# Kernel tuning notes

Hardware: AMD Instinct MI355X
Metric: run time of the kernel (lower is better)

## Reference

```python
import jax, jax.numpy as jnp
import numpy as np

EMBED_DIM = 1024
NUM_HEADS = 16
HEAD_DIM = EMBED_DIM // NUM_HEADS


def setup_inputs() -> dict:
    key = jax.random.key(0)
    ks = jax.random.split(key, 9)
    B, S, D = 2, 2048, EMBED_DIM
    scale = 1.0 / np.sqrt(D)
    x = jax.random.normal(ks[0], (B, S, D), dtype=jnp.float32)
    # nn.Linear weights are stored as (out, in); y = x @ W.T + b
    Wq = jax.random.uniform(ks[1], (D, D), jnp.float32, -scale, scale)
    bq = jax.random.uniform(ks[2], (D,), jnp.float32, -scale, scale)
    Wk = jax.random.uniform(ks[3], (D, D), jnp.float32, -scale, scale)
    bk = jax.random.uniform(ks[4], (D,), jnp.float32, -scale, scale)
    Wv = jax.random.uniform(ks[5], (D, D), jnp.float32, -scale, scale)
    bv = jax.random.uniform(ks[6], (D,), jnp.float32, -scale, scale)
    Wo = jax.random.uniform(ks[7], (D, D), jnp.float32, -scale, scale)
    bo = jax.random.uniform(ks[8], (D,), jnp.float32, -scale, scale)
    return {"x": x, "Wq": Wq, "bq": bq, "Wk": Wk, "bk": bk,
            "Wv": Wv, "bv": bv, "Wo": Wo, "bo": bo}


def reference(x, Wq, bq, Wk, bk, Wv, bv, Wo, bo):
    B, S, D = x.shape
    H, Hd = NUM_HEADS, HEAD_DIM

    def split_heads(t):  # [B,S,D] -> [B,H,S,Hd]
        return t.reshape(B, S, H, Hd).transpose(0, 2, 1, 3)

    Q = split_heads(x @ Wq.T + bq)
    K = split_heads(x @ Wk.T + bk)
    V = split_heads(x @ Wv.T + bv)

    scores = jnp.einsum('bhqd,bhkd->bhqk', Q, K) / jnp.sqrt(
        jnp.asarray(Hd, dtype=x.dtype))
    attn = jax.nn.softmax(scores, axis=-1)
    out = jnp.einsum('bhqk,bhkd->bhqd', attn, V)  # [B,H,S,Hd]
    out = out.transpose(0, 2, 1, 3).reshape(B, S, D)
    return out @ Wo.T + bo
```

## Files before the change

kernel.cpp:

```cpp
#include <hip/hip_runtime.h>
#include <hip/hip_bf16.h>
#include <stdint.h>

typedef __attribute__((ext_vector_type(8))) short short8;
typedef __attribute__((ext_vector_type(4))) float f32x4;
typedef unsigned short u16;
typedef unsigned int u32;

static constexpr int S = 2048;
static constexpr int H = 16;
static constexpr int HD = 64;

__device__ __forceinline__ float fast_exp2(float x){
  return __builtin_amdgcn_exp2f(x);
}

__device__ __forceinline__ u16 f2bf(float f){
  union { float f; u32 u; } x; x.f = f;
  u32 r = x.u + 0x7fffu + ((x.u >> 16) & 1u);
  return (u16)(r >> 16);
}

__device__ __forceinline__ u32 cvt_pk_bf16(float lo, float hi){
  u32 r;
  asm("v_cvt_pk_bf16_f32 %0, %1, %2" : "=v"(r) : "v"(lo), "v"(hi));
  return r;
}

__global__ __launch_bounds__(256) void cast_all(const float* __restrict__ x,
                                                const float* __restrict__ Wq,
                                                const float* __restrict__ Wk,
                                                const float* __restrict__ Wv,
                                                const float* __restrict__ Wo,
                                                u16* __restrict__ xb,
                                                u16* __restrict__ Wb){
  int i = (blockIdx.x * 256 + threadIdx.x) * 4;
  const float* s; u16* d; int off;
  if (i < 4194304){
    s = x; d = xb; off = i;
  } else {
    int j = i - 4194304;
    int w = j >> 20;
    s = (w == 0) ? Wq : (w == 1) ? Wk : (w == 2) ? Wv : Wo;
    d = Wb + (w << 20);
    off = j & 1048575;
  }
  float4 v = *(const float4*)(s + off);
  ushort4 o;
  o.x = f2bf(v.x); o.y = f2bf(v.y); o.z = f2bf(v.z); o.w = f2bf(v.w);
  *(ushort4*)(d + off) = o;
}

__device__ __forceinline__ void gload_lds16(const void* g, void* lds_uniform){
  __builtin_amdgcn_global_load_lds(
      (const __attribute__((address_space(1))) u32*)g,
      (__attribute__((address_space(3))) u32*)lds_uniform,
      16, 0, 0);
}

__global__ __launch_bounds__(256) void gemm_qkv(const u16* __restrict__ A,
                                                const u16* __restrict__ Wall,
                                                const float* __restrict__ b0p,
                                                const float* __restrict__ b1p,
                                                const float* __restrict__ b2p,
                                                u16* __restrict__ obf){
  __shared__ __align__(16) u16 As[128*32];
  __shared__ __align__(16) u16 Bs[128*32];

  const int tid  = threadIdx.x;
  const int lane = tid & 63;
  const int wid  = tid >> 6;
  const int wm = wid >> 1, wn = wid & 1;
  const int l4 = lane >> 4, l15 = lane & 15;

  const int L = blockIdx.x + 8*blockIdx.y + 256*blockIdx.z;
  const int W = (L & 7)*96 + (L >> 3);
  const int z = W >> 8;
  const int rem = W & 255;
  const int n0 = (rem & 7) * 128;
  const int m0 = (rem >> 3) * 128;

  const u16* Bw = Wall + (size_t)z * (1024*1024);
  const float* bias = (z == 0) ? b0p : ((z == 1) ? b1p : b2p);

  f32x4 acc[4][4];
  #pragma unroll
  for (int m=0;m<4;m++)
    #pragma unroll
    for (int n=0;n<4;n++) acc[m][n] = (f32x4){0.f,0.f,0.f,0.f};

  const char* Ab = (const char*)A  + (size_t)m0 * 2048;
  const char* Bb = (const char*)Bw + (size_t)n0 * 2048;
  char* AsB = (char*)As;
  char* BsB = (char*)Bs;

  int ldsu[2], row_[2], col_[2];
  #pragma unroll
  for (int p=0;p<2;p++){
    ldsu[p] = wid*1024 + p*4096;
    int b = ldsu[p] + lane*16;
    row_[p] = b >> 6;
    col_[p] = b & 63;
  }

  for (int kt = 0; kt < 32; ++kt){
    const int kb = kt * 64;
    #pragma unroll
    for (int p=0;p<2;p++){
      gload_lds16(Ab + (size_t)row_[p]*2048 + kb + col_[p], AsB + ldsu[p]);
      gload_lds16(Bb + (size_t)row_[p]*2048 + kb + col_[p], BsB + ldsu[p]);
    }
    __syncthreads();

    short8 af[4], bfr[4];
    const int kcol = 8 * l4;
    #pragma unroll
    for (int m=0;m<4;m++)
      af[m] = *(const short8*)&As[(wm*64 + m*16 + l15)*32 + kcol];
    #pragma unroll
    for (int n=0;n<4;n++)
      bfr[n] = *(const short8*)&Bs[(wn*64 + n*16 + l15)*32 + kcol];

    #pragma unroll
    for (int m=0;m<4;m++)
      #pragma unroll
      for (int n=0;n<4;n++)
        acc[m][n] = __builtin_amdgcn_mfma_f32_16x16x32_bf16(af[m], bfr[n], acc[m][n], 0,0,0);

    __syncthreads();
  }

  #pragma unroll
  for (int m=0;m<4;m++){
    const int rgb = m0 + wm*64 + m*16 + 4*l4;
    #pragma unroll
    for (int n=0;n<4;n++){
      const int cg = n0 + wn*64 + n*16 + l15;
      const float bb = bias[cg];
      const int bi = rgb >> 11, si = rgb & 2047;
      const int hi = cg >> 6,  hd = cg & 63;
      if (z == 2){
        u16* outz = obf + (size_t)2 * 4194304u;
        ushort4 o;
        o.x = f2bf(acc[m][n][0] + bb);
        o.y = f2bf(acc[m][n][1] + bb);
        o.z = f2bf(acc[m][n][2] + bb);
        o.w = f2bf(acc[m][n][3] + bb);
        *(ushort4*)&outz[(((size_t)(bi*16 + hi))*64 + hd)*2048 + si] = o;
      } else {
        u16* outz = obf + (size_t)z * 4194304u;
        const float sc = (z == 0) ? 0.18033688011112042f : 1.0f;
        #pragma unroll
        for (int r=0;r<4;r++)
          outz[(((size_t)(bi*16 + hi))*2048 + (si + r))*64 + hd] =
              f2bf((acc[m][n][r] + bb) * sc);
      }
    }
  }
}

__global__ __launch_bounds__(256) void gemm_out(const u16* __restrict__ A,
                                                const u16* __restrict__ Wo,
                                                const float* __restrict__ bo,
                                                float* __restrict__ ofp){
  __shared__ __align__(16) u16 As[64*32];
  __shared__ __align__(16) u16 Bs[128*32];

  const int tid  = threadIdx.x;
  const int lane = tid & 63;
  const int wid  = tid >> 6;
  const int wm = wid >> 1, wn = wid & 1;
  const int l4 = lane >> 4, l15 = lane & 15;

  const int L = blockIdx.x + 8*blockIdx.y;
  const int W = (L & 7)*64 + (L >> 3);
  const int n0 = (W & 7) * 128;
  const int m0 = (W >> 3) * 64;

  f32x4 acc[2][4];
  #pragma unroll
  for (int m=0;m<2;m++)
    #pragma unroll
    for (int n=0;n<4;n++) acc[m][n] = (f32x4){0.f,0.f,0.f,0.f};

  const char* Ab = (const char*)A  + (size_t)m0 * 2048;
  const char* Bb = (const char*)Wo + (size_t)n0 * 2048;
  char* AsB = (char*)As;
  char* BsB = (char*)Bs;

  const int ldsuA = wid*1024;
  int rowA, colA;
  { int b = ldsuA + lane*16; rowA = b >> 6; colA = b & 63; }
  int ldsuB[2], rowB[2], colB[2];
  #pragma unroll
  for (int p=0;p<2;p++){
    ldsuB[p] = wid*2048 + p*1024;
    int b = ldsuB[p] + lane*16;
    rowB[p] = b >> 6; colB[p] = b & 63;
  }

  for (int kt = 0; kt < 32; ++kt){
    const int kb = kt * 64;
    gload_lds16(Ab + (size_t)rowA*2048 + kb + colA, AsB + ldsuA);
    #pragma unroll
    for (int p=0;p<2;p++)
      gload_lds16(Bb + (size_t)rowB[p]*2048 + kb + colB[p], BsB + ldsuB[p]);
    __syncthreads();

    short8 af[2], bfr[4];
    const int kcol = 8 * l4;
    #pragma unroll
    for (int m=0;m<2;m++)
      af[m] = *(const short8*)&As[(wm*32 + m*16 + l15)*32 + kcol];
    #pragma unroll
    for (int n=0;n<4;n++)
      bfr[n] = *(const short8*)&Bs[(wn*64 + n*16 + l15)*32 + kcol];

    #pragma unroll
    for (int m=0;m<2;m++)
      #pragma unroll
      for (int n=0;n<4;n++)
        acc[m][n] = __builtin_amdgcn_mfma_f32_16x16x32_bf16(af[m], bfr[n], acc[m][n], 0,0,0);

    __syncthreads();
  }

  #pragma unroll
  for (int m=0;m<2;m++){
    const int rgb = m0 + wm*32 + m*16 + 4*l4;
    #pragma unroll
    for (int n=0;n<4;n++){
      const int cg = n0 + wn*64 + n*16 + l15;
      const float bb = bo[cg];
      #pragma unroll
      for (int r=0;r<4;r++)
        ofp[(size_t)(rgb + r)*1024 + cg] = acc[m][n][r] + bb;
    }
  }
}

__global__ __launch_bounds__(256) void attn_fwd(const u16* __restrict__ Qg,
                                                const u16* __restrict__ Kg,
                                                const u16* __restrict__ Vtg,
                                                u16* __restrict__ Og){
  __shared__ __align__(16) u16 Ks[2*64*64];
  __shared__ __align__(16) u16 Vs[2*64*64];
  __shared__ __align__(16) u16 Ps[4*16*64];

  const int tid  = threadIdx.x;
  const int lane = tid & 63;
  const int wid  = tid >> 6;
  const int l4 = lane >> 4, l15 = lane & 15;
  const int swz = l15 & 7;

  const int L = blockIdx.x + 32*blockIdx.y;
  const int W = (L & 7)*128 + (L >> 3);
  const int qb = W & 31;
  const int bh = W >> 5;
  const size_t hoff = (size_t)bh * (S * HD);

  short8 aq0, aq1;
  {
    const u16* qp = Qg + hoff + (size_t)(qb*64 + wid*16 + l15) * HD;
    aq0 = *(const short8*)(qp + 8*l4);
    aq1 = *(const short8*)(qp + 32 + 8*l4);
  }

  const float FM = 12.0f;
  float lr = 0.f;
  f32x4 oacc[4];
  #pragma unroll
  for (int hb=0;hb<4;hb++) oacc[hb] = (f32x4){0.f,0.f,0.f,0.f};

  const char* Kb = (const char*)(Kg  + hoff);
  const char* Vb = (const char*)(Vtg + hoff);
  char* KsB = (char*)Ks;
  char* VsB = (char*)Vs;
  char* PsB = (char*)Ps + wid*2048;

  int ldsu[2], srcK[2], srcV[2];
  #pragma unroll
  for (int p=0;p<2;p++){
    ldsu[p] = wid*2048 + p*1024;
    int b   = ldsu[p] + lane*16;
    int row = b >> 7, cc = (b >> 4) & 7;
    int ccs = cc ^ (row & 7);
    srcK[p] = row*128  + (ccs << 4);
    srcV[p] = row*4096 + (ccs << 4);
  }

  #pragma unroll
  for (int p=0;p<2;p++){
    gload_lds16(Kb + srcK[p], KsB + ldsu[p]);
    gload_lds16(Vb + srcV[p], VsB + ldsu[p]);
  }
  __syncthreads();

  #pragma unroll 2
  for (int kt = 0; kt < S/64; ++kt){
    const int cur = kt & 1;
    if (kt + 1 < S/64){
      const int nxt = cur ^ 1;
      const char* Ksrc = Kb + (size_t)(kt+1)*8192;
      const char* Vsrc = Vb + (size_t)(kt+1)*128;
      #pragma unroll
      for (int p=0;p<2;p++){
        gload_lds16(Ksrc + srcK[p], KsB + nxt*8192 + ldsu[p]);
        gload_lds16(Vsrc + srcV[p], VsB + nxt*8192 + ldsu[p]);
      }
    }

    const char* KsC = KsB + cur*8192;
    const char* VsC = VsB + cur*8192;

    f32x4 sacc[4];
    __builtin_amdgcn_s_setprio(1);
    #pragma unroll
    for (int nb=0;nb<4;nb++){
      const int krow = nb*16 + l15;
      short8 k0 = *(const short8*)(KsC + krow*128 + ((l4 ^ swz) << 4));
      short8 k1 = *(const short8*)(KsC + krow*128 + (((4 + l4) ^ swz) << 4));
      f32x4 zz = (f32x4){0.f,0.f,0.f,0.f};
      zz = __builtin_amdgcn_mfma_f32_16x16x32_bf16(k0, aq0, zz, 0,0,0);
      zz = __builtin_amdgcn_mfma_f32_16x16x32_bf16(k1, aq1, zz, 0,0,0);
      sacc[nb] = zz;
    }
    __builtin_amdgcn_s_setprio(0);

    float rs = 0.f;
    #pragma unroll
    for (int nb=0;nb<4;nb++)
      #pragma unroll
      for (int r=0;r<4;r++){
        float p = fast_exp2(sacc[nb][r] - FM);
        sacc[nb][r] = p;
        rs += p;
      }
    lr += rs;

    #pragma unroll
    for (int nb=0;nb<4;nb++){
      u32 lo = cvt_pk_bf16(sacc[nb][0], sacc[nb][1]);
      u32 hi = cvt_pk_bf16(sacc[nb][2], sacc[nb][3]);
      const int chunk = nb*2 + (l4 >> 1);
      const int sub   = (l4 & 1) * 8;
      *(uint2*)(PsB + l15*128 + ((chunk ^ swz) << 4) + sub) = make_uint2(lo, hi);
    }

    __builtin_amdgcn_s_setprio(1);
    #pragma unroll
    for (int ks=0;ks<2;ks++){
      short8 ap = *(const short8*)(PsB + l15*128 + (((ks*4 + l4) ^ swz) << 4));
      #pragma unroll
      for (int hb=0;hb<4;hb++){
        const int vrow = hb*16 + l15;
        short8 bv = *(const short8*)(VsC + vrow*128 + (((ks*4 + l4) ^ swz) << 4));
        oacc[hb] = __builtin_amdgcn_mfma_f32_16x16x32_bf16(ap, bv, oacc[hb], 0,0,0);
      }
    }
    __builtin_amdgcn_s_setprio(0);
    __syncthreads();
  }

  lr += __shfl_xor(lr, 16, 64);
  lr += __shfl_xor(lr, 32, 64);
  float inv[4];
  #pragma unroll
  for (int r=0;r<4;r++){
    float lq = __shfl(lr, 4*l4 + r, 64);
    inv[r] = 1.0f / lq;
  }
  const int b = bh >> 4, h = bh & 15;
  #pragma unroll
  for (int hb=0;hb<4;hb++){
    #pragma unroll
    for (int r=0;r<4;r++){
      const int si = qb*64 + wid*16 + 4*l4 + r;
      const float v = oacc[hb][r] * inv[r];
      Og[(((size_t)(b*S + si))*H + h)*HD + hb*16 + l15] = f2bf(v);
    }
  }
}

extern "C" void kernel_launch(void* const* d_in, const int* in_sizes, int n_in,
                              void* d_out, int out_size, void* d_ws, size_t ws_size,
                              hipStream_t stream) {
  const float* x  = (const float*)d_in[0];
  const float* Wq = (const float*)d_in[1];
  const float* bq = (const float*)d_in[2];
  const float* Wk = (const float*)d_in[3];
  const float* bk = (const float*)d_in[4];
  const float* Wv = (const float*)d_in[5];
  const float* bv = (const float*)d_in[6];
  const float* Wo = (const float*)d_in[7];
  const float* bo = (const float*)d_in[8];

  char* ws = (char*)d_ws;
  u16* xb  = (u16*)(ws);
  u16* Wb  = (u16*)(ws + (size_t)8*1024*1024);
  u16* QKV = (u16*)(ws + (size_t)16*1024*1024);
  u16* AO  = (u16*)(ws + (size_t)40*1024*1024);
  float* out = (float*)d_out;

  cast_all<<<8192, 256, 0, stream>>>(x, Wq, Wk, Wv, Wo, xb, Wb);

  dim3 g1(8, 32, 3);
  gemm_qkv<<<g1, 256, 0, stream>>>(xb, Wb, bq, bk, bv, QKV);

  dim3 g2(32, 32, 1);
  attn_fwd<<<g2, 256, 0, stream>>>(QKV, QKV + 4194304, QKV + 2*4194304, AO);

  dim3 g3(8, 64, 1);
  gemm_out<<<g3, 256, 0, stream>>>(AO, Wb + 3145728, bo, out);
}
```

Baseline: 130.7 us.

## Double-buffer LDS tiles in QKV and output GEMMs with MFMA priority boost

Both projection GEMMs now hold two LDS tile buffers. The loads for the next K-tile are issued before the MFMAs on the current tile, which keeps one barrier per iteration and lets global-to-LDS traffic overlap with matrix math. The MFMA block is also wrapped in s_setprio to favour the compute waves. The cost is double the shared memory per block, which may lower occupancy, and correctness relies on the end-of-loop barrier draining the async loads.

```diff
diff --git a/kernel.cpp b/kernel.cpp
--- a/kernel.cpp
+++ b/kernel.cpp
@@ -64,8 +64,8 @@
                                                 const float* __restrict__ b1p,
                                                 const float* __restrict__ b2p,
                                                 u16* __restrict__ obf){
-  __shared__ __align__(16) u16 As[128*32];
-  __shared__ __align__(16) u16 Bs[128*32];
+  __shared__ __align__(16) u16 As[2*128*32];
+  __shared__ __align__(16) u16 Bs[2*128*32];
 
   const int tid  = threadIdx.x;
   const int lane = tid & 63;
@@ -103,29 +103,43 @@
     col_[p] = b & 63;
   }
 
+  #pragma unroll
+  for (int p=0;p<2;p++){
+    gload_lds16(Ab + (size_t)row_[p]*2048 + col_[p], AsB + ldsu[p]);
+    gload_lds16(Bb + (size_t)row_[p]*2048 + col_[p], BsB + ldsu[p]);
+  }
+  __syncthreads();
+
   for (int kt = 0; kt < 32; ++kt){
-    const int kb = kt * 64;
-    #pragma unroll
-    for (int p=0;p<2;p++){
-      gload_lds16(Ab + (size_t)row_[p]*2048 + kb + col_[p], AsB + ldsu[p]);
-      gload_lds16(Bb + (size_t)row_[p]*2048 + kb + col_[p], BsB + ldsu[p]);
-    }
-    __syncthreads();
+    const int cur = kt & 1;
+    if (kt + 1 < 32){
+      const int nxt = cur ^ 1;
+      const int kb = (kt + 1) * 64;
+      #pragma unroll
+      for (int p=0;p<2;p++){
+        gload_lds16(Ab + (size_t)row_[p]*2048 + kb + col_[p], AsB + nxt*8192 + ldsu[p]);
+        gload_lds16(Bb + (size_t)row_[p]*2048 + kb + col_[p], BsB + nxt*8192 + ldsu[p]);
+      }
+    }
+    const u16* Asc = (const u16*)(AsB + cur*8192);
+    const u16* Bsc = (const u16*)(BsB + cur*8192);
 
     short8 af[4], bfr[4];
     const int kcol = 8 * l4;
     #pragma unroll
     for (int m=0;m<4;m++)
-      af[m] = *(const short8*)&As[(wm*64 + m*16 + l15)*32 + kcol];
+      af[m] = *(const short8*)&Asc[(wm*64 + m*16 + l15)*32 + kcol];
     #pragma unroll
     for (int n=0;n<4;n++)
-      bfr[n] = *(const short8*)&Bs[(wn*64 + n*16 + l15)*32 + kcol];
-
+      bfr[n] = *(const short8*)&Bsc[(wn*64 + n*16 + l15)*32 + kcol];
+
+    __builtin_amdgcn_s_setprio(1);
     #pragma unroll
     for (int m=0;m<4;m++)
       #pragma unroll
       for (int n=0;n<4;n++)
         acc[m][n] = __builtin_amdgcn_mfma_f32_16x16x32_bf16(af[m], bfr[n], acc[m][n], 0,0,0);
+    __builtin_amdgcn_s_setprio(0);
 
     __syncthreads();
   }
@@ -163,8 +177,8 @@
                                                 const u16* __restrict__ Wo,
                                                 const float* __restrict__ bo,
                                                 float* __restrict__ ofp){
-  __shared__ __align__(16) u16 As[64*32];
-  __shared__ __align__(16) u16 Bs[128*32];
+  __shared__ __align__(16) u16 As[2*64*32];
+  __shared__ __align__(16) u16 Bs[2*128*32];
 
   const int tid  = threadIdx.x;
   const int lane = tid & 63;
@@ -199,28 +213,41 @@
     rowB[p] = b >> 6; colB[p] = b & 63;
   }
 
+  gload_lds16(Ab + (size_t)rowA*2048 + colA, AsB + ldsuA);
+  #pragma unroll
+  for (int p=0;p<2;p++)
+    gload_lds16(Bb + (size_t)rowB[p]*2048 + colB[p], BsB + ldsuB[p]);
+  __syncthreads();
+
   for (int kt = 0; kt < 32; ++kt){
-    const int kb = kt * 64;
-    gload_lds16(Ab + (size_t)rowA*2048 + kb + colA, AsB + ldsuA);
-    #pragma unroll
-    for (int p=0;p<2;p++)
-      gload_lds16(Bb + (size_t)rowB[p]*2048 + kb + colB[p], BsB + ldsuB[p]);
-    __syncthreads();
+    const int cur = kt & 1;
+    if (kt + 1 < 32){
+      const int nxt = cur ^ 1;
+      const int kb = (kt + 1) * 64;
+      gload_lds16(Ab + (size_t)rowA*2048 + kb + colA, AsB + nxt*4096 + ldsuA);
+      #pragma unroll
+      for (int p=0;p<2;p++)
+        gload_lds16(Bb + (size_t)rowB[p]*2048 + kb + colB[p], BsB + nxt*8192 + ldsuB[p]);
+    }
+    const u16* Asc = (const u16*)(AsB + cur*4096);
+    const u16* Bsc = (const u16*)(BsB + cur*8192);
 
     short8 af[2], bfr[4];
     const int kcol = 8 * l4;
     #pragma unroll
     for (int m=0;m<2;m++)
-      af[m] = *(const short8*)&As[(wm*32 + m*16 + l15)*32 + kcol];
+      af[m] = *(const short8*)&Asc[(wm*32 + m*16 + l15)*32 + kcol];
     #pragma unroll
     for (int n=0;n<4;n++)
-      bfr[n] = *(const short8*)&Bs[(wn*64 + n*16 + l15)*32 + kcol];
-
+      bfr[n] = *(const short8*)&Bsc[(wn*64 + n*16 + l15)*32 + kcol];
+
+    __builtin_amdgcn_s_setprio(1);
     #pragma unroll
     for (int m=0;m<2;m++)
       #pragma unroll
       for (int n=0;n<4;n++)
         acc[m][n] = __builtin_amdgcn_mfma_f32_16x16x32_bf16(af[m], bfr[n], acc[m][n], 0,0,0);
+    __builtin_amdgcn_s_setprio(0);
 
     __syncthreads();
   }
```

Result: faster. 123.0 us (-5.9%).
